# Optimization experiments

Hardware: AMD Instinct MI355X
Metric: run time of the kernel (lower is better)

Reference implementation:

```python
import jax, jax.numpy as jnp
import numpy as np

DIM = 512
NUM_GROUPS = 32
NUM_HEADS = 8
EPS = 1e-5


def group_norm(x, gamma, beta):
    # x: (B, C, H, W); normalize over (C//G, H, W) per group
    B, C, H, W = x.shape
    g = x.reshape(B, NUM_GROUPS, -1)
    mean = g.mean(axis=2, keepdims=True)
    var = g.var(axis=2, keepdims=True)
    g = (g - mean) * jax.lax.rsqrt(var + EPS)
    x = g.reshape(B, C, H, W)
    return x * gamma[None, :, None, None] + beta[None, :, None, None]


def setup_inputs() -> dict:
    key = jax.random.key(0)
    ks = jax.random.split(key, 7)
    B, C, H, W = 16, DIM, 32, 32
    x = jax.random.normal(ks[0], (B, C, H, W), dtype=jnp.float32)
    gamma = jnp.ones((C,), dtype=jnp.float32)
    beta = jnp.zeros((C,), dtype=jnp.float32)
    s_in = 1.0 / np.sqrt(C)
    w_qkv = jax.random.normal(ks[1], (3 * C, C), dtype=jnp.float32) * s_in
    b_qkv = jnp.zeros((3 * C,), dtype=jnp.float32)
    w_proj = jax.random.normal(ks[2], (C, C), dtype=jnp.float32) * s_in
    b_proj = jnp.zeros((C,), dtype=jnp.float32)
    return {"x": x, "gamma": gamma, "beta": beta, "w_qkv": w_qkv,
            "b_qkv": b_qkv, "w_proj": w_proj, "b_proj": b_proj}


def reference(x, gamma, beta, w_qkv, b_qkv, w_proj, b_proj):
    B, C, H, W = x.shape
    nh = NUM_HEADS
    c3 = 3 * C // nh          # per-head qkv channels (3 * head_dim)
    dh = C // nh              # head_dim
    scale = C ** (-0.5)       # NOTE: source scales by full dim, not head_dim

    h = group_norm(x, gamma, beta)

    # 1x1 conv qkv projection: (B, 3C, H, W)
    qkv = jnp.einsum('bchw,oc->bohw', h, w_qkv) + b_qkv[None, :, None, None]

    # rearrange 'b (head c) h w -> (b head) (h w) c'
    qkv = qkv.reshape(B, nh, c3, H, W)
    qkv = qkv.transpose(0, 1, 3, 4, 2).reshape(B * nh, H * W, c3)
    q, k, v = jnp.split(qkv, 3, axis=2)   # each (B*nh, HW, dh)

    score = jnp.einsum('bnc,bmc->bnm', q, k * scale)   # (B*nh, HW, HW)
    attn = jax.nn.softmax(score, axis=2)
    out = jnp.einsum('bnm,bmc->bnc', attn, v)          # (B*nh, HW, dh)

    # rearrange '(head b) (h w) c -> b (head c) h w'  (NOTE head-major, as in source)
    out = out.reshape(nh, B, H, W, dh)
    out = out.transpose(1, 0, 4, 2, 3).reshape(B, C, H, W)

    out = jnp.einsum('bchw,oc->bohw', out, w_proj) + b_proj[None, :, None, None]
    return out + x
```

## Files before the change

### kernel.cpp

```cpp
#include <hip/hip_runtime.h>
#include <stdint.h>

typedef __bf16 bf16;
typedef __attribute__((ext_vector_type(4))) float f32x4;
typedef __attribute__((ext_vector_type(8))) __bf16 bf16x8;
typedef __attribute__((ext_vector_type(4))) __bf16 bf16x4;

#define NB 16
#define CH 512
#define HWS 1024
#define NHEAD 8
#define DH 64
#define O3 1536
#define LDP 72
#define CPQ 136
#define CPF 132

__global__ void prep(const float* __restrict__ x, float* __restrict__ stats,
                     const float* __restrict__ wq, const float* __restrict__ wp,
                     bf16* __restrict__ wq_b, bf16* __restrict__ wp_b) {
    int bx = blockIdx.x;
    if (bx < 512) {
        int b = bx >> 5, g = bx & 31;
        const float4* p = (const float4*)(x + ((size_t)(b * CH + g * 16)) * HWS);
        float s = 0.f, ss = 0.f;
        for (int i = threadIdx.x; i < 4096; i += 256) {
            float4 v = p[i];
            s  += v.x + v.y + v.z + v.w;
            ss += v.x*v.x + v.y*v.y + v.z*v.z + v.w*v.w;
        }
        for (int off = 32; off; off >>= 1) {
            s  += __shfl_xor(s,  off, 64);
            ss += __shfl_xor(ss, off, 64);
        }
        __shared__ float red[8];
        int w = threadIdx.x >> 6;
        if ((threadIdx.x & 63) == 0) { red[w*2] = s; red[w*2+1] = ss; }
        __syncthreads();
        if (threadIdx.x == 0) {
            float S  = red[0] + red[2] + red[4] + red[6];
            float SS = red[1] + red[3] + red[5] + red[7];
            float mean = S * (1.f/16384.f);
            float var  = SS * (1.f/16384.f) - mean*mean;
            stats[bx*2]   = mean;
            stats[bx*2+1] = rsqrtf(var + 1e-5f);
        }
    } else {
        int i = (bx - 512) * 256 + threadIdx.x;
        if (i < O3*CH) wq_b[i] = (bf16)wq[i];
        else           wp_b[i - O3*CH] = (bf16)wp[i - O3*CH];
    }
}

__global__ void gn_apply_t(const float* __restrict__ x, const float* __restrict__ stats,
                           const float* __restrict__ gamma, const float* __restrict__ beta,
                           bf16* __restrict__ hT) {
    __shared__ float tile[32][33];
    int bx = blockIdx.x;
    int b = bx >> 9;
    int rem = bx & 511;
    int ct = rem >> 5, nt = rem & 31;
    int tx = threadIdx.x & 31, ty = threadIdx.x >> 5;
    #pragma unroll
    for (int r = 0; r < 4; ++r) {
        int c = ct*32 + ty + r*8;
        int n = nt*32 + tx;
        float v = x[((size_t)(b * CH + c)) * HWS + n];
        int g = c >> 4;
        float mean = stats[(b*32+g)*2], rstd = stats[(b*32+g)*2+1];
        tile[ty + r*8][tx] = (v - mean) * rstd * gamma[c] + beta[c];
    }
    __syncthreads();
    #pragma unroll
    for (int r = 0; r < 4; ++r) {
        int n = nt*32 + ty + r*8;
        int c = ct*32 + tx;
        hT[((size_t)(b * HWS + n)) * CH + c] = (bf16)tile[tx][ty + r*8];
    }
}

__global__ __launch_bounds__(256, 3)
void qkv_gemm(const bf16* __restrict__ W, const bf16* __restrict__ hT,
              const float* __restrict__ bias, bf16* __restrict__ qkv,
              bf16* __restrict__ vT) {
    __shared__ __align__(16) bf16 SMEM[2*128*LDP];
    bf16* As = SMEM;
    bf16* Bs = SMEM + 128*LDP;
    int bx = blockIdx.x;
    int po = bx >> 7, qo = bx & 127;
    int obase = po*128, bnbase = qo*128;
    int tid = threadIdx.x;
    int lane = tid & 63, w = tid >> 6;
    int quad = lane >> 4, l15 = lane & 15;
    int wm = w >> 1, wn = w & 1;

    f32x4 acc[4][4] = {};
    for (int k0 = 0; k0 < 512; k0 += 64) {
        #pragma unroll
        for (int r = 0; r < 4; ++r) {
            int c = r*256 + tid;
            int row = c >> 3, dc = c & 7;
            uint4 va = *(const uint4*)(W  + ((size_t)(obase + row)) * 512 + k0 + dc*8);
            *(uint4*)(&As[row*LDP + dc*8]) = va;
            uint4 vb = *(const uint4*)(hT + ((size_t)(bnbase + row)) * 512 + k0 + dc*8);
            *(uint4*)(&Bs[row*LDP + dc*8]) = vb;
        }
        __syncthreads();
        #pragma unroll
        for (int ks = 0; ks < 2; ++ks) {
            bf16x8 af[4], bfv[4];
            #pragma unroll
            for (int mt = 0; mt < 4; ++mt)
                af[mt] = *(const bf16x8*)(&As[(wm*64 + mt*16 + l15)*LDP + ks*32 + quad*8]);
            #pragma unroll
            for (int nt = 0; nt < 4; ++nt)
                bfv[nt] = *(const bf16x8*)(&Bs[(wn*64 + nt*16 + l15)*LDP + ks*32 + quad*8]);
            #pragma unroll
            for (int mt = 0; mt < 4; ++mt)
                #pragma unroll
                for (int nt = 0; nt < 4; ++nt)
                    acc[mt][nt] = __builtin_amdgcn_mfma_f32_16x16x32_bf16(af[mt], bfv[nt], acc[mt][nt], 0, 0, 0);
        }
        __syncthreads();
    }

    bf16* Cs = SMEM;
    int b = bnbase >> 10;
    int nbase = bnbase & 1023;
    #pragma unroll
    for (int mt = 0; mt < 4; ++mt) {
        int o0 = obase + wm*64 + mt*16 + quad*4;
        float4 bb = *(const float4*)(bias + o0);
        int c192 = o0 % 192;
        bool isV = (c192 >= 128);
        int h = o0 / 192;
        int d0 = c192 - 128;
        #pragma unroll
        for (int nt = 0; nt < 4; ++nt) {
            int bn_l = wn*64 + nt*16 + l15;
            bf16x4 v;
            v[0] = (bf16)(acc[mt][nt][0] + bb.x);
            v[1] = (bf16)(acc[mt][nt][1] + bb.y);
            v[2] = (bf16)(acc[mt][nt][2] + bb.z);
            v[3] = (bf16)(acc[mt][nt][3] + bb.w);
            *(bf16x4*)(&Cs[bn_l*CPQ + (o0 - obase)]) = v;
            if (isV) {
                int key = nbase + bn_l;
                size_t vb_ = ((size_t)((b*8 + h)*64 + d0)) * HWS + key;
                vT[vb_]          = v[0];
                vT[vb_ + HWS]    = v[1];
                vT[vb_ + 2*HWS]  = v[2];
                vT[vb_ + 3*HWS]  = v[3];
            }
        }
    }
    __syncthreads();
    #pragma unroll
    for (int p = 0; p < 8; ++p) {
        int bn_l = p*16 + (tid >> 4);
        int o8 = (tid & 15) * 8;
        if ((obase + o8) % 192 < 128) {
            uint4 v = *(const uint4*)(&Cs[bn_l*CPQ + o8]);
            *(uint4*)(qkv + ((size_t)(bnbase + bn_l)) * O3 + obase + o8) = v;
        }
    }
}

__global__ __launch_bounds__(256, 4)
void flash_attn(const bf16* __restrict__ qkv, const bf16* __restrict__ vT,
                bf16* __restrict__ A2) {
    __shared__ __align__(16) bf16 Ks[64*LDP];
    __shared__ __align__(16) bf16 Vs[64*LDP];
    __shared__ __align__(16) bf16 Ps[4][32*LDP];
    int bx = blockIdx.x;
    int g = bx & 127, qt = bx >> 7;
    int b = g >> 3, h = g & 7;
    int tid = threadIdx.x, lane = tid & 63, w = tid >> 6;
    int quad = lane >> 4, l15 = lane & 15;
    const float kLog2 = 0.04419417382415922f * 1.44269504088896341f;

    bf16x8 aq[2][2];
    #pragma unroll
    for (int mt = 0; mt < 2; ++mt) {
        int qrow = qt*128 + w*32 + mt*16 + l15;
        const bf16* qb = qkv + ((size_t)(b * HWS + qrow)) * O3 + h*192;
        aq[mt][0] = *(const bf16x8*)(qb + quad*8);
        aq[mt][1] = *(const bf16x8*)(qb + 32 + quad*8);
    }

    f32x4 acc[2][4] = {};
    float L[2] = {0.f, 0.f};

    int r0 = tid >> 3, d0 = (tid & 7) * 8;
    int r1 = r0 + 32;
    const bf16* kp0 = qkv + ((size_t)(b * HWS + r0)) * O3 + h*192 + 64 + d0;
    const bf16* kp1 = qkv + ((size_t)(b * HWS + r1)) * O3 + h*192 + 64 + d0;
    const bf16* vp0 = vT + ((size_t)(g * DH + r0)) * HWS + d0;
    const bf16* vp1 = vT + ((size_t)(g * DH + r1)) * HWS + d0;
    bf16* ksd0 = &Ks[r0*LDP + d0];
    bf16* ksd1 = &Ks[r1*LDP + d0];
    bf16* vsd0 = &Vs[r0*LDP + d0];
    bf16* vsd1 = &Vs[r1*LDP + d0];

    uint4 ka = *(const uint4*)(kp0);
    uint4 kb = *(const uint4*)(kp1);
    uint4 va = *(const uint4*)(vp0);
    uint4 vb = *(const uint4*)(vp1);

    for (int kt = 0; kt < 16; ++kt) {
        __syncthreads();
        *(uint4*)ksd0 = ka;
        *(uint4*)ksd1 = kb;
        *(uint4*)vsd0 = va;
        *(uint4*)vsd1 = vb;
        __syncthreads();
        if (kt < 15) {
            size_t ko = (size_t)(kt+1) * 64 * O3;
            size_t vo = (size_t)(kt+1) * 64;
            ka = *(const uint4*)(kp0 + ko);
            kb = *(const uint4*)(kp1 + ko);
            va = *(const uint4*)(vp0 + vo);
            vb = *(const uint4*)(vp1 + vo);
        }

        #pragma unroll
        for (int nt = 0; nt < 4; ++nt) {
            bf16x8 ak0 = *(const bf16x8*)(&Ks[(nt*16 + l15)*LDP + quad*8]);
            bf16x8 ak1 = *(const bf16x8*)(&Ks[(nt*16 + l15)*LDP + 32 + quad*8]);
            #pragma unroll
            for (int mt = 0; mt < 2; ++mt) {
                f32x4 z = {};
                z = __builtin_amdgcn_mfma_f32_16x16x32_bf16(ak0, aq[mt][0], z, 0, 0, 0);
                z = __builtin_amdgcn_mfma_f32_16x16x32_bf16(ak1, aq[mt][1], z, 0, 0, 0);
                bf16x4 p;
                #pragma unroll
                for (int r = 0; r < 4; ++r) {
                    float e = exp2f(z[r] * kLog2);
                    L[mt] += e;
                    p[r] = (bf16)e;
                }
                *(bf16x4*)(&Ps[w][(mt*16 + l15)*LDP + nt*16 + quad*4]) = p;
            }
        }
        bf16x8 ap[2][2];
        #pragma unroll
        for (int mt = 0; mt < 2; ++mt) {
            ap[mt][0] = *(const bf16x8*)(&Ps[w][(mt*16 + l15)*LDP + quad*8]);
            ap[mt][1] = *(const bf16x8*)(&Ps[w][(mt*16 + l15)*LDP + 32 + quad*8]);
        }
        #pragma unroll
        for (int dt = 0; dt < 4; ++dt) {
            bf16x8 bv0 = *(const bf16x8*)(&Vs[(dt*16 + l15)*LDP + quad*8]);
            bf16x8 bv1 = *(const bf16x8*)(&Vs[(dt*16 + l15)*LDP + 32 + quad*8]);
            #pragma unroll
            for (int mt = 0; mt < 2; ++mt) {
                acc[mt][dt] = __builtin_amdgcn_mfma_f32_16x16x32_bf16(ap[mt][0], bv0, acc[mt][dt], 0, 0, 0);
                acc[mt][dt] = __builtin_amdgcn_mfma_f32_16x16x32_bf16(ap[mt][1], bv1, acc[mt][dt], 0, 0, 0);
            }
        }
    }

    float Linv[2][4];
    #pragma unroll
    for (int mt = 0; mt < 2; ++mt) {
        float Lf = L[mt];
        Lf += __shfl_xor(Lf, 16, 64);
        Lf += __shfl_xor(Lf, 32, 64);
        #pragma unroll
        for (int r = 0; r < 4; ++r)
            Linv[mt][r] = 1.f / __shfl(Lf, quad*4 + r, 64);
    }

    __syncthreads();
    #pragma unroll
    for (int mt = 0; mt < 2; ++mt)
        #pragma unroll
        for (int dt = 0; dt < 4; ++dt)
            #pragma unroll
            for (int r = 0; r < 4; ++r)
                Ps[w][(mt*16 + quad*4 + r)*LDP + dt*16 + l15] = (bf16)(acc[mt][dt][r] * Linv[mt][r]);

    int bp = g & 15;
    int hp = g >> 4;
    #pragma unroll
    for (int cc = 0; cc < 4; ++cc) {
        int c = cc*64 + lane;
        int row = c >> 3, dc = c & 7;
        uint4 v = *(const uint4*)(&Ps[w][row*LDP + dc*8]);
        size_t idx = ((size_t)(bp * HWS + qt*128 + w*32 + row)) * CH + hp*64 + dc*8;
        *(uint4*)(A2 + idx) = v;
    }
}

__global__ __launch_bounds__(256, 3)
void proj_gemm(const bf16* __restrict__ A2, const bf16* __restrict__ Wp,
               const float* __restrict__ bias, const float* __restrict__ x,
               float* __restrict__ out) {
    __shared__ __align__(16) bf16 SMEM[2*128*LDP];
    bf16* As = SMEM;
    bf16* Bs = SMEM + 128*LDP;
    int bx = blockIdx.x;
    int po = bx >> 7, qo = bx & 127;
    int obase = po*128, bnbase = qo*128;
    int tid = threadIdx.x;
    int lane = tid & 63, w = tid >> 6;
    int quad = lane >> 4, l15 = lane & 15;
    int wm = w >> 1, wn = w & 1;

    f32x4 acc[4][4] = {};
    for (int k0 = 0; k0 < 512; k0 += 64) {
        #pragma unroll
        for (int r = 0; r < 4; ++r) {
            int c = r*256 + tid;
            int row = c >> 3, dc = c & 7;
            uint4 va = *(const uint4*)(A2 + ((size_t)(bnbase + row)) * 512 + k0 + dc*8);
            *(uint4*)(&As[row*LDP + dc*8]) = va;
            uint4 vb = *(const uint4*)(Wp + ((size_t)(obase + row)) * 512 + k0 + dc*8);
            *(uint4*)(&Bs[row*LDP + dc*8]) = vb;
        }
        __syncthreads();
        #pragma unroll
        for (int ks = 0; ks < 2; ++ks) {
            bf16x8 af[4], bfv[4];
            #pragma unroll
            for (int mt = 0; mt < 4; ++mt)
                af[mt] = *(const bf16x8*)(&As[(wm*64 + mt*16 + l15)*LDP + ks*32 + quad*8]);
            #pragma unroll
            for (int nt = 0; nt < 4; ++nt)
                bfv[nt] = *(const bf16x8*)(&Bs[(wn*64 + nt*16 + l15)*LDP + ks*32 + quad*8]);
            #pragma unroll
            for (int mt = 0; mt < 4; ++mt)
                #pragma unroll
                for (int nt = 0; nt < 4; ++nt)
                    acc[mt][nt] = __builtin_amdgcn_mfma_f32_16x16x32_bf16(af[mt], bfv[nt], acc[mt][nt], 0, 0, 0);
        }
        __syncthreads();
    }

    float* Cf = (float*)SMEM;
    int bb = bnbase >> 10;
    int nbase = bnbase & 1023;
    #pragma unroll
    for (int hh = 0; hh < 2; ++hh) {
        if (wm == hh) {
            #pragma unroll
            for (int mt = 0; mt < 4; ++mt)
                #pragma unroll
                for (int nt = 0; nt < 4; ++nt)
                    #pragma unroll
                    for (int r = 0; r < 4; ++r)
                        Cf[(mt*16 + quad*4 + r)*CPF + wn*64 + nt*16 + l15] = acc[mt][nt][r];
        }
        __syncthreads();
        #pragma unroll
        for (int p = 0; p < 4; ++p) {
            int ol = p*32 + (tid >> 3);
            int nl0 = (tid & 7) * 8;
            int o = obase + ol;
            float bv = bias[o];
            #pragma unroll
            for (int jj = 0; jj < 2; ++jj) {
                int nl = nl0 + jj*4;
                size_t idx = ((size_t)(bb * CH + o)) * HWS + nbase + hh*64 + nl;
                float4 xr = *(const float4*)(x + idx);
                float4 res;
                res.x = Cf[(nl+0)*CPF + ol] + bv + xr.x;
                res.y = Cf[(nl+1)*CPF + ol] + bv + xr.y;
                res.z = Cf[(nl+2)*CPF + ol] + bv + xr.z;
                res.w = Cf[(nl+3)*CPF + ol] + bv + xr.w;
                *(float4*)(out + idx) = res;
            }
        }
        __syncthreads();
    }
}

extern "C" void kernel_launch(void* const* d_in, const int* in_sizes, int n_in,
                              void* d_out, int out_size, void* d_ws, size_t ws_size,
                              hipStream_t stream) {
    const float* x      = (const float*)d_in[0];
    const float* gamma  = (const float*)d_in[1];
    const float* beta   = (const float*)d_in[2];
    const float* w_qkv  = (const float*)d_in[3];
    const float* b_qkv  = (const float*)d_in[4];
    const float* w_proj = (const float*)d_in[5];
    const float* b_proj = (const float*)d_in[6];
    float* out = (float*)d_out;

    char* ws = (char*)d_ws;
    float* stats = (float*)(ws + 0);
    bf16*  wq_b  = (bf16*)(ws + 4096);
    bf16*  wp_b  = (bf16*)(ws + 1576960);
    bf16*  hT    = (bf16*)(ws + 2101248);
    bf16*  qkv   = (bf16*)(ws + 18878464);
    bf16*  vT    = (bf16*)(ws + 69210112);
    bf16*  A2    = hT;

    prep       <<<4608, 256, 0, stream>>>(x, stats, w_qkv, w_proj, wq_b, wp_b);
    gn_apply_t <<<8192, 256, 0, stream>>>(x, stats, gamma, beta, hT);
    qkv_gemm   <<<1536, 256, 0, stream>>>(wq_b, hT, b_qkv, qkv, vT);
    flash_attn <<<1024, 256, 0, stream>>>(qkv, vT, A2);
    proj_gemm  <<<512,  256, 0, stream>>>(A2, wp_b, b_proj, x, out);
}
```

Before: 220.2 us.

## Double-buffer K/V tiles in flash attention with XOR-swizzled LDS layout

K and V shared-memory tiles become double-buffered, so the barrier at the start of each key tile is removed and only one sync per iteration remains. The padded LDP stride is replaced by an unpadded 64-wide stride with an XOR swizzle on the 8-element column chunk to avoid bank conflicts. The extra LDS use lowers the occupancy hint from 4 to 3 blocks per CU, which may reduce latency hiding.

```diff
diff --git a/kernel.cpp b/kernel.cpp
--- a/kernel.cpp
+++ b/kernel.cpp
@@ -12,6 +12,7 @@
 #define NHEAD 8
 #define DH 64
 #define O3 1536
+#define KLP 64
 #define LDP 72
 #define CPQ 136
 #define CPF 132
@@ -166,17 +167,18 @@
     }
 }
 
-__global__ __launch_bounds__(256, 4)
+__global__ __launch_bounds__(256, 3)
 void flash_attn(const bf16* __restrict__ qkv, const bf16* __restrict__ vT,
                 bf16* __restrict__ A2) {
-    __shared__ __align__(16) bf16 Ks[64*LDP];
-    __shared__ __align__(16) bf16 Vs[64*LDP];
+    __shared__ __align__(16) bf16 Kd[2][64*KLP];
+    __shared__ __align__(16) bf16 Vd[2][64*KLP];
     __shared__ __align__(16) bf16 Ps[4][32*LDP];
     int bx = blockIdx.x;
     int g = bx & 127, qt = bx >> 7;
     int b = g >> 3, h = g & 7;
     int tid = threadIdx.x, lane = tid & 63, w = tid >> 6;
     int quad = lane >> 4, l15 = lane & 15;
+    int x7 = l15 & 7;
     const float kLog2 = 0.04419417382415922f * 1.44269504088896341f;
 
     bf16x8 aq[2][2];
@@ -191,16 +193,14 @@
     f32x4 acc[2][4] = {};
     float L[2] = {0.f, 0.f};
 
-    int r0 = tid >> 3, d0 = (tid & 7) * 8;
+    int r0 = tid >> 3, dc = tid & 7, d0 = dc * 8;
     int r1 = r0 + 32;
+    int sOff0 = r0*KLP + ((dc ^ (r0 & 7)) * 8);
+    int sOff1 = r1*KLP + ((dc ^ (r0 & 7)) * 8);
     const bf16* kp0 = qkv + ((size_t)(b * HWS + r0)) * O3 + h*192 + 64 + d0;
     const bf16* kp1 = qkv + ((size_t)(b * HWS + r1)) * O3 + h*192 + 64 + d0;
     const bf16* vp0 = vT + ((size_t)(g * DH + r0)) * HWS + d0;
     const bf16* vp1 = vT + ((size_t)(g * DH + r1)) * HWS + d0;
-    bf16* ksd0 = &Ks[r0*LDP + d0];
-    bf16* ksd1 = &Ks[r1*LDP + d0];
-    bf16* vsd0 = &Vs[r0*LDP + d0];
-    bf16* vsd1 = &Vs[r1*LDP + d0];
 
     uint4 ka = *(const uint4*)(kp0);
     uint4 kb = *(const uint4*)(kp1);
@@ -208,11 +208,12 @@
     uint4 vb = *(const uint4*)(vp1);
 
     for (int kt = 0; kt < 16; ++kt) {
-        __syncthreads();
-        *(uint4*)ksd0 = ka;
-        *(uint4*)ksd1 = kb;
-        *(uint4*)vsd0 = va;
-        *(uint4*)vsd1 = vb;
+        bf16* Kb = &Kd[kt & 1][0];
+        bf16* Vb = &Vd[kt & 1][0];
+        *(uint4*)(Kb + sOff0) = ka;
+        *(uint4*)(Kb + sOff1) = kb;
+        *(uint4*)(Vb + sOff0) = va;
+        *(uint4*)(Vb + sOff1) = vb;
         __syncthreads();
         if (kt < 15) {
             size_t ko = (size_t)(kt+1) * 64 * O3;
@@ -225,8 +226,9 @@
 
         #pragma unroll
         for (int nt = 0; nt < 4; ++nt) {
-            bf16x8 ak0 = *(const bf16x8*)(&Ks[(nt*16 + l15)*LDP + quad*8]);
-            bf16x8 ak1 = *(const bf16x8*)(&Ks[(nt*16 + l15)*LDP + 32 + quad*8]);
+            int ro = (nt*16 + l15)*KLP;
+            bf16x8 ak0 = *(const bf16x8*)(&Kb[ro + ((quad ^ x7)*8)]);
+            bf16x8 ak1 = *(const bf16x8*)(&Kb[ro + (((4 + quad) ^ x7)*8)]);
             #pragma unroll
             for (int mt = 0; mt < 2; ++mt) {
                 f32x4 z = {};
@@ -250,8 +252,9 @@
         }
         #pragma unroll
         for (int dt = 0; dt < 4; ++dt) {
-            bf16x8 bv0 = *(const bf16x8*)(&Vs[(dt*16 + l15)*LDP + quad*8]);
-            bf16x8 bv1 = *(const bf16x8*)(&Vs[(dt*16 + l15)*LDP + 32 + quad*8]);
+            int ro = (dt*16 + l15)*KLP;
+            bf16x8 bv0 = *(const bf16x8*)(&Vb[ro + ((quad ^ x7)*8)]);
+            bf16x8 bv1 = *(const bf16x8*)(&Vb[ro + (((4 + quad) ^ x7)*8)]);
             #pragma unroll
             for (int mt = 0; mt < 2; ++mt) {
                 acc[mt][dt] = __builtin_amdgcn_mfma_f32_16x16x32_bf16(ap[mt][0], bv0, acc[mt][dt], 0, 0, 0);
@@ -285,9 +288,9 @@
     #pragma unroll
     for (int cc = 0; cc < 4; ++cc) {
         int c = cc*64 + lane;
-        int row = c >> 3, dc = c & 7;
-        uint4 v = *(const uint4*)(&Ps[w][row*LDP + dc*8]);
-        size_t idx = ((size_t)(bp * HWS + qt*128 + w*32 + row)) * CH + hp*64 + dc*8;
+        int row = c >> 3, dcc = c & 7;
+        uint4 v = *(const uint4*)(&Ps[w][row*LDP + dcc*8]);
+        size_t idx = ((size_t)(bp * HWS + qt*128 + w*32 + row)) * CH + hp*64 + dcc*8;
         *(uint4*)(A2 + idx) = v;
     }
 }
```

New measurement: 220.8 us. Within noise of the previous version (+0.3%).
